# Kernel tuning notes

Measured on AMD Instinct MI355X. Metric: run time of the kernel, lower is better.

The kernel has to match this reference:

```python
import jax, jax.numpy as jnp
import numpy as np

N = 524288
B, F, H, W = 2, 4, 64, 512
S = B * F * H * W  # dense voxel segment space
EPS = 1e-5


def _bn(x, g, b):
    # BatchNorm1d in training mode: normalize over the point dim with biased var
    m = x.mean(0)
    v = jnp.mean((x - m) ** 2, 0)
    return (x - m) / jnp.sqrt(v + EPS) * g + b


def setup_inputs() -> dict:
    key = jax.random.key(0)
    ks = jax.random.split(key, 20)
    pts = jax.random.normal(ks[0], (N, 4), dtype=jnp.float32) * 10.0
    bcol = jax.random.randint(ks[1], (N, 1), 0, B)
    fcol = jax.random.randint(ks[2], (N, 1), 0, F)
    hcol = jax.random.randint(ks[3], (N, 1), 0, H)
    wcol = jax.random.randint(ks[4], (N, 1), 0, W)
    coors = jnp.concatenate([bcol, fcol, hcol, wcol], -1).astype(jnp.int32)
    # original reads batch_size/frame_size from coors[-1]
    coors = coors.at[-1].set(jnp.array([B - 1, F - 1, H - 1, W - 1], dtype=jnp.int32))
    s = 0.02
    p = {
        'pre_gamma': jnp.ones((8,), jnp.float32),
        'pre_beta': jnp.zeros((8,), jnp.float32),
        'W1': jax.random.normal(ks[5], (8, 64), jnp.float32) * s,
        'g1': jnp.ones((64,), jnp.float32), 'b1': jnp.zeros((64,), jnp.float32),
        'W2': jax.random.normal(ks[6], (64, 128), jnp.float32) * s,
        'g2': jnp.ones((128,), jnp.float32), 'b2': jnp.zeros((128,), jnp.float32),
        'W3': jax.random.normal(ks[7], (128, 256), jnp.float32) * s,
        'g3': jnp.ones((256,), jnp.float32), 'b3': jnp.zeros((256,), jnp.float32),
        'W4': jax.random.normal(ks[8], (256, 256), jnp.float32) * s,
        'b4': jnp.zeros((256,), jnp.float32),
        'Wc': jax.random.normal(ks[9], (256, 64), jnp.float32) * s,
        'bc': jnp.zeros((64,), jnp.float32),
    }
    return {'pts': pts, 'pts_coors': coors, **p}


def reference(pts, pts_coors, pre_gamma, pre_beta, W1, g1, b1, W2, g2, b2,
              W3, g3, b3, W4, b4, Wc, bc):
    c = pts_coors
    lin = ((c[:, 0] * F + c[:, 1]) * H + c[:, 2]) * W + c[:, 3]  # (N,)
    counts = jax.ops.segment_sum(jnp.ones((pts.shape[0],), pts.dtype), lin, num_segments=S)
    # with_distance
    dist = jnp.linalg.norm(pts[:, :3], axis=1, keepdims=True)
    # with_cluster_center: scatter_mean then gather
    vsum = jax.ops.segment_sum(pts, lin, num_segments=S)
    vmean = vsum / jnp.clip(counts, 1.0)[:, None]
    f_cluster = pts[:, :3] - vmean[lin][:, :3]
    feats = jnp.concatenate([pts, dist, f_cluster], -1)  # (N, 8)
    feats = _bn(feats, pre_gamma, pre_beta)  # pre_norm
    x = jax.nn.relu(_bn(feats @ W1, g1, b1))
    x = jax.nn.relu(_bn(x @ W2, g2, b2))
    x = jax.nn.relu(_bn(x @ W3, g3, b3))
    point_feats = x @ W4 + b4  # (N, 256)
    # scatter_max over voxels
    seg = jax.ops.segment_max(point_feats, lin, num_segments=S)
    mask = (counts > 0)[:, None]
    voxel_feats = jnp.where(mask, seg, 0.0)
    comp = jax.nn.relu(voxel_feats @ Wc + bc)
    comp = jnp.where(mask, comp, 0.0)  # empty voxels stay zero in stack_frame
    stack = comp.reshape(B, F, H, W, -1)  # (B, F, H, W, Cc)
    residual = jnp.concatenate([stack[:, -1] - stack[:, f] for f in range(F - 1)], -1)
    residual_img = jnp.transpose(residual, (0, 3, 1, 2))  # (B, C, H, W)
    return residual_img
```

## Files before the change

### kernel.cpp

```cpp
#include <hip/hip_runtime.h>
#include <hip/hip_bf16.h>
#include <stdint.h>

typedef unsigned int u32;
typedef unsigned short u16;
typedef __attribute__((ext_vector_type(8))) short bf16x8;
typedef __attribute__((ext_vector_type(4))) float f32x4;

#define NPTS 524288
#define FF 4
#define HH 64
#define WW 512
#define SS 262144
#define EPSV 1e-5f
#define NB 8192
#define RCAP 80
#define VCAP 80

__device__ __forceinline__ float bf2f(u16 h){ return __uint_as_float(((u32)h)<<16); }
__device__ __forceinline__ u16 f2bf(float f){
  u32 u = __float_as_uint(f);
  return (u16)((u + 0x7FFFu + ((u>>16)&1u)) >> 16);
}

__device__ __forceinline__ void point_feats(int p, const float* __restrict__ pts,
    const u32* __restrict__ lin, const u32* __restrict__ counts,
    const float* __restrict__ vsum, float f[8], u32* vout){
  float4 pt = ((const float4*)pts)[p];
  u32 v = lin[p];
  float cnt = fmaxf((float)counts[v], 1.0f);
  float inv = 1.0f/cnt;
  float mx = vsum[v*3+0]*inv, my = vsum[v*3+1]*inv, mz = vsum[v*3+2]*inv;
  float dist = sqrtf(pt.x*pt.x + pt.y*pt.y + pt.z*pt.z);
  f[0]=pt.x; f[1]=pt.y; f[2]=pt.z; f[3]=pt.w; f[4]=dist;
  f[5]=pt.x-mx; f[6]=pt.y-my; f[7]=pt.z-mz;
  *vout = v;
}

__global__ __launch_bounds__(256) void k_lin(const float* __restrict__ pts,
                                             const int* __restrict__ coors,
                                             u32* __restrict__ lin,
                                             u32* __restrict__ counts,
                                             float* __restrict__ vsum){
  int p = blockIdx.x*256 + threadIdx.x;
  int4 c = ((const int4*)coors)[p];
  u32 v = ((u32)((c.x*FF + c.y)*HH + c.z))*WW + (u32)c.w;
  lin[p] = v;
  atomicAdd(&counts[v], 1u);
  float4 pt = ((const float4*)pts)[p];
  atomicAdd(&vsum[v*3+0], pt.x);
  atomicAdd(&vsum[v*3+1], pt.y);
  atomicAdd(&vsum[v*3+2], pt.z);
}

__global__ __launch_bounds__(256) void k_scan_a(const u32* __restrict__ counts,
                                                u32* __restrict__ blockSums){
  __shared__ u32 lds[256];
  int b = blockIdx.x, t = threadIdx.x;
  uint4 c4 = ((const uint4*)counts)[b*256 + t];
  lds[t] = c4.x + c4.y + c4.z + c4.w;
  __syncthreads();
  for(int s=128; s>0; s>>=1){ if(t<s) lds[t] += lds[t+s]; __syncthreads(); }
  if(t==0) blockSums[b] = lds[0];
}

__global__ void k_scan_b(u32* blockSums){
  if(threadIdx.x==0){
    u32 run = 0;
    for(int i=0;i<256;i++){ u32 v = blockSums[i]; blockSums[i] = run; run += v; }
  }
}

__global__ __launch_bounds__(256) void k_scan_c(const u32* __restrict__ counts,
                                                const u32* __restrict__ blockSums,
                                                u32* __restrict__ offsets,
                                                u32* __restrict__ cursor){
  __shared__ u32 lds[256];
  int b = blockIdx.x, t = threadIdx.x;
  uint4 c4 = ((const uint4*)counts)[b*256 + t];
  u32 mysum = c4.x + c4.y + c4.z + c4.w;
  lds[t] = mysum;
  __syncthreads();
  for(int d=1; d<256; d<<=1){
    u32 v = (t>=d) ? lds[t-d] : 0u;
    __syncthreads();
    lds[t] += v;
    __syncthreads();
  }
  u32 off = blockSums[b] + (t>0 ? lds[t-1] : 0u);
  u32 base = (u32)(b*1024 + t*4);
  offsets[base+0]=off; cursor[base+0]=off; off += c4.x;
  offsets[base+1]=off; cursor[base+1]=off; off += c4.y;
  offsets[base+2]=off; cursor[base+2]=off; off += c4.z;
  offsets[base+3]=off; cursor[base+3]=off; off += c4.w;
  if(base+4 == SS) offsets[SS] = off;
}

__global__ __launch_bounds__(256) void k_scatter(const u32* __restrict__ lin,
                                                 u32* __restrict__ cursor,
                                                 u32* __restrict__ order){
  int p = blockIdx.x*256 + threadIdx.x;
  u32 v = lin[p];
  u32 pos = atomicAdd(&cursor[v], 1u);
  order[pos] = p;
}

__global__ __launch_bounds__(256) void k_prep(const float* __restrict__ W2,
    const float* __restrict__ W3, const float* __restrict__ W4,
    const float* __restrict__ Wc,
    u16* __restrict__ W2t, u16* __restrict__ W3t, u16* __restrict__ W4t,
    u16* __restrict__ Wct){
  int i = blockIdx.x*256 + threadIdx.x;
  if(i < 8192){
    int k = i >> 7, n = i & 127;
    W2t[n*64 + k] = f2bf(W2[i]);
  } else if(i < 8192+32768){
    int j = i - 8192;
    int k = j >> 8, n = j & 255;
    W3t[n*128 + k] = f2bf(W3[j]);
  } else if(i < 8192+32768+65536){
    int j = i - (8192+32768);
    int k = j >> 8, n = j & 255;
    W4t[n*256 + k] = f2bf(W4[j]);
  } else if(i < 8192+32768+65536+16384){
    int j = i - (8192+32768+65536);
    int k = j >> 6, n = j & 63;
    Wct[n*256 + k] = f2bf(Wc[j]);
  }
}

__global__ __launch_bounds__(256) void k_stats0(const float* __restrict__ pts,
    const u32* __restrict__ lin, const u32* __restrict__ counts,
    const float* __restrict__ vsum, float* __restrict__ sum0, float* __restrict__ sq0){
  int p = blockIdx.x*256 + threadIdx.x;
  float f[8]; u32 v;
  point_feats(p, pts, lin, counts, vsum, f, &v);
  __shared__ float lsum[4][8], lsq[4][8];
  int lane = threadIdx.x & 63, wv = threadIdx.x >> 6;
  #pragma unroll
  for(int c=0;c<8;c++){
    float s = f[c], q = f[c]*f[c];
    #pragma unroll
    for(int d=32; d; d>>=1){ s += __shfl_xor(s,d); q += __shfl_xor(q,d); }
    if(lane==0){ lsum[wv][c]=s; lsq[wv][c]=q; }
  }
  __syncthreads();
  if(threadIdx.x<8){
    float s=0.f,q=0.f;
    for(int g=0;g<4;g++){ s+=lsum[g][threadIdx.x]; q+=lsq[g][threadIdx.x]; }
    atomicAdd(&sum0[threadIdx.x], s);
    atomicAdd(&sq0[threadIdx.x], q);
  }
}

__global__ void k_fold(const float* __restrict__ sum, const float* __restrict__ sq,
                       const float* __restrict__ g, const float* __restrict__ b,
                       float* __restrict__ a, float* __restrict__ c, int C){
  int i = blockIdx.x*64 + threadIdx.x;
  if(i < C){
    float m = sum[i]*(1.0f/NPTS);
    float v = sq[i]*(1.0f/NPTS) - m*m;
    v = fmaxf(v, 0.0f);
    float ai = g[i] / sqrtf(v + EPSV);
    a[i] = ai;
    c[i] = b[i] - m*ai;
  }
}

__global__ __launch_bounds__(256) void k_stats1(const float* __restrict__ pts,
    const u32* __restrict__ lin, const u32* __restrict__ counts,
    const float* __restrict__ vsum,
    const float* __restrict__ a0, const float* __restrict__ c0,
    const float* __restrict__ W1, float* __restrict__ sum1, float* __restrict__ sq1){
  __shared__ float ws[4][64], wq[4][64];
  int t = threadIdx.x;
  int p = blockIdx.x*256 + t;
  float f[8]; u32 v;
  point_feats(p, pts, lin, counts, vsum, f, &v);
  float y0[8];
  #pragma unroll
  for(int k=0;k<8;k++) y0[k] = a0[k]*f[k] + c0[k];
  float z[64];
  #pragma unroll
  for(int j=0;j<64;j++){
    float s=0.f;
    #pragma unroll
    for(int k=0;k<8;k++) s += y0[k]*W1[k*64+j];
    z[j]=s;
  }
  int lane = t&63, wv = t>>6;
  float ks=0.f, kq=0.f;
  #pragma unroll
  for(int c=0;c<64;c++){
    float s=z[c], q=z[c]*z[c];
    #pragma unroll
    for(int d=1; d<64; d<<=1){ s+=__shfl_xor(s,d); q+=__shfl_xor(q,d); }
    if(lane==c){ ks=s; kq=q; }
  }
  ws[wv][lane]=ks; wq[wv][lane]=kq;
  __syncthreads();
  if(t<64){
    float S=ws[0][t]+ws[1][t]+ws[2][t]+ws[3][t];
    float Q=wq[0][t]+wq[1][t]+wq[2][t]+wq[3][t];
    atomicAdd(&sum1[t],S); atomicAdd(&sq1[t],Q);
  }
}

__global__ __launch_bounds__(256,2) void k_mstats2(
    const float* __restrict__ pts, const u32* __restrict__ lin,
    const u32* __restrict__ counts, const float* __restrict__ vsum,
    const float* __restrict__ a0, const float* __restrict__ c0,
    const float* __restrict__ a1, const float* __restrict__ c1,
    const float* __restrict__ W1, const u16* __restrict__ W2t,
    float* __restrict__ sum2, float* __restrict__ sq2){
  __shared__ u16 T1[256*72];
  int tid = threadIdx.x, lane = tid&63, wid = tid>>6, l15 = lane&15, lg = lane>>4;
  float s2[2] = {0.f,0.f}, q2[2] = {0.f,0.f};

  for(int cch=0; cch<4; cch++){
    int p = blockIdx.x*1024 + cch*256 + tid;
    float f[8]; u32 v;
    point_feats(p, pts, lin, counts, vsum, f, &v);
    float y0[8];
    #pragma unroll
    for(int k=0;k<8;k++) y0[k] = a0[k]*f[k] + c0[k];
    u32 pk[32];
    #pragma unroll
    for(int jj=0;jj<32;jj++){
      float s0=0.f, s1=0.f;
      #pragma unroll
      for(int k=0;k<8;k++){ s0 += y0[k]*W1[k*64+2*jj]; s1 += y0[k]*W1[k*64+2*jj+1]; }
      float v0f = fmaxf(a1[2*jj]*s0   + c1[2*jj],   0.f);
      float v1f = fmaxf(a1[2*jj+1]*s1 + c1[2*jj+1], 0.f);
      pk[jj] = (u32)f2bf(v0f) | ((u32)f2bf(v1f)<<16);
    }
    __syncthreads();
    {
      uint4* dst = (uint4*)&T1[tid*72];
      #pragma unroll
      for(int q=0;q<8;q++) dst[q] = make_uint4(pk[4*q],pk[4*q+1],pk[4*q+2],pk[4*q+3]);
    }
    __syncthreads();
    #pragma unroll
    for(int ci=0; ci<2; ci++){
      int ch = (wid + 4*ci)*16 + l15;
      const u16* wb = W2t + (size_t)ch*64 + lg*8;
      bf16x8 b0 = *(const bf16x8*)(wb);
      bf16x8 b1 = *(const bf16x8*)(wb + 32);
      for(int rt=0; rt<16; rt++){
        const u16* ap = T1 + (rt*16 + l15)*72 + lg*8;
        bf16x8 af0 = *(const bf16x8*)(ap);
        bf16x8 af1 = *(const bf16x8*)(ap + 32);
        f32x4 acc = {0.f,0.f,0.f,0.f};
        acc = __builtin_amdgcn_mfma_f32_16x16x32_bf16(af0, b0, acc, 0,0,0);
        acc = __builtin_amdgcn_mfma_f32_16x16x32_bf16(af1, b1, acc, 0,0,0);
        #pragma unroll
        for(int i=0;i<4;i++){ s2[ci] += acc[i]; q2[ci] += acc[i]*acc[i]; }
      }
    }
  }
  #pragma unroll
  for(int ci=0; ci<2; ci++){
    float s = s2[ci], q = q2[ci];
    s += __shfl_xor(s,16); s += __shfl_xor(s,32);
    q += __shfl_xor(q,16); q += __shfl_xor(q,32);
    if(lg == 0){
      int ch = (wid + 4*ci)*16 + l15;
      atomicAdd(&sum2[ch], s);
      atomicAdd(&sq2[ch], q);
    }
  }
}

__global__ __launch_bounds__(256,1) void k_chain2(
    const float* __restrict__ pts, const u32* __restrict__ lin,
    const u32* __restrict__ counts, const float* __restrict__ vsum,
    const u32* __restrict__ order,
    const float* __restrict__ a0, const float* __restrict__ c0,
    const float* __restrict__ a1, const float* __restrict__ c1,
    const float* __restrict__ a2, const float* __restrict__ c2,
    const float* __restrict__ W1, const u16* __restrict__ W2t,
    const u16* __restrict__ W3t,
    u32* __restrict__ y2s,
    float* __restrict__ sum3, float* __restrict__ sq3){
  __shared__ u16 T1[256*72];
  __shared__ u16 T2[256*136];
  int tid = threadIdx.x, lane = tid&63, wid = tid>>6, l15 = lane&15, lg = lane>>4;
  float s3[4] = {0.f,0.f,0.f,0.f}, q3[4] = {0.f,0.f,0.f,0.f};

  for(int cch=0; cch<4; cch++){
    int rr = blockIdx.x*1024 + cch*256 + tid;
    int p = (int)order[rr];
    float f[8]; u32 v;
    point_feats(p, pts, lin, counts, vsum, f, &v);
    float y0[8];
    #pragma unroll
    for(int k=0;k<8;k++) y0[k] = a0[k]*f[k] + c0[k];
    u32 pk[32];
    #pragma unroll
    for(int jj=0;jj<32;jj++){
      float s0=0.f, s1=0.f;
      #pragma unroll
      for(int k=0;k<8;k++){ s0 += y0[k]*W1[k*64+2*jj]; s1 += y0[k]*W1[k*64+2*jj+1]; }
      float v0f = fmaxf(a1[2*jj]*s0   + c1[2*jj],   0.f);
      float v1f = fmaxf(a1[2*jj+1]*s1 + c1[2*jj+1], 0.f);
      pk[jj] = (u32)f2bf(v0f) | ((u32)f2bf(v1f)<<16);
    }
    __syncthreads();
    {
      uint4* dst = (uint4*)&T1[tid*72];
      #pragma unroll
      for(int q=0;q<8;q++) dst[q] = make_uint4(pk[4*q],pk[4*q+1],pk[4*q+2],pk[4*q+3]);
    }
    __syncthreads();
    #pragma unroll
    for(int ci=0; ci<2; ci++){
      int ch = (wid + 4*ci)*16 + l15;
      const u16* wb = W2t + (size_t)ch*64 + lg*8;
      bf16x8 b0 = *(const bf16x8*)(wb);
      bf16x8 b1 = *(const bf16x8*)(wb + 32);
      float a2v = a2[ch], c2v = c2[ch];
      for(int rt=0; rt<16; rt++){
        const u16* ap = T1 + (rt*16 + l15)*72 + lg*8;
        bf16x8 af0 = *(const bf16x8*)(ap);
        bf16x8 af1 = *(const bf16x8*)(ap + 32);
        f32x4 acc = {0.f,0.f,0.f,0.f};
        acc = __builtin_amdgcn_mfma_f32_16x16x32_bf16(af0, b0, acc, 0,0,0);
        acc = __builtin_amdgcn_mfma_f32_16x16x32_bf16(af1, b1, acc, 0,0,0);
        int rbase = rt*16 + lg*4;
        #pragma unroll
        for(int i=0;i<4;i++)
          T2[(rbase+i)*136 + ch] = f2bf(fmaxf(a2v*acc[i] + c2v, 0.f));
      }
    }
    __syncthreads();
    {
      const u32* T2w = (const u32*)T2;
      u32 base = (u32)blockIdx.x*1024u + (u32)cch*256u;
      for(int i=tid; i<256*64; i+=256){
        int row = i>>6, w = i&63;
        y2s[(size_t)(base+row)*64 + w] = T2w[row*68 + w];
      }
    }
    #pragma unroll
    for(int ci=0; ci<4; ci++){
      int ch = (wid + 4*ci)*16 + l15;
      const u16* wb = W3t + (size_t)ch*128 + lg*8;
      bf16x8 b[4];
      #pragma unroll
      for(int ks=0; ks<4; ks++) b[ks] = *(const bf16x8*)(wb + ks*32);
      for(int rt=0; rt<16; rt++){
        const u16* ap = T2 + (rt*16 + l15)*136 + lg*8;
        f32x4 acc = {0.f,0.f,0.f,0.f};
        #pragma unroll
        for(int ks=0; ks<4; ks++){
          bf16x8 af = *(const bf16x8*)(ap + ks*32);
          acc = __builtin_amdgcn_mfma_f32_16x16x32_bf16(af, b[ks], acc, 0,0,0);
        }
        #pragma unroll
        for(int i=0;i<4;i++){ s3[ci] += acc[i]; q3[ci] += acc[i]*acc[i]; }
      }
    }
  }
  #pragma unroll
  for(int ci=0; ci<4; ci++){
    float s = s3[ci], q = q3[ci];
    s += __shfl_xor(s,16); s += __shfl_xor(s,32);
    q += __shfl_xor(q,16); q += __shfl_xor(q,32);
    if(lg == 0){
      int ch = (wid + 4*ci)*16 + l15;
      atomicAdd(&sum3[ch], s);
      atomicAdd(&sq3[ch], q);
    }
  }
}

__global__ __launch_bounds__(512,4) void k_mega5(
    const u32* __restrict__ offsets, const u32* __restrict__ y2s,
    const float* __restrict__ a3, const float* __restrict__ c3,
    const u16* __restrict__ W3t, const u16* __restrict__ W4t,
    const u16* __restrict__ Wct,
    const float* __restrict__ b4, const float* __restrict__ bc,
    u16* __restrict__ comp){
  __shared__ __align__(16) char SM[65664];
  u16* T3  = (u16*)(SM);
  u16* T2s = (u16*)(SM + 42240);
  u16* Tz  = (u16*)(SM + 42240);
  u16* TA  = (u16*)(SM + 53760);
  u32* vst = (u32*)(SM + 65280);
  u32* hdr = (u32*)(SM + 65616);

  int tid = threadIdx.x, lane = tid & 63, wid = tid >> 6;
  int l15 = lane & 15, lg = lane >> 4;
  int cg = wid & 3, rh = wid >> 2;
  int nvt = rh ? 2 : 3, vt0 = rh ? 3 : 0;

  if(tid == 0){
    u32 t0 = (u32)blockIdx.x * 64u;
    u32 lo=0, hi=SS;
    while(lo<hi){ u32 mid=(lo+hi)>>1; if(offsets[mid] < t0) lo=mid+1; else hi=mid; }
    u32 vlo = lo, vhi;
    if(blockIdx.x == NB-1) vhi = SS;
    else {
      u32 t1 = t0 + 64u;
      lo = vlo; hi = SS;
      while(lo<hi){ u32 mid=(lo+hi)>>1; if(offsets[mid] < t1) lo=mid+1; else hi=mid; }
      vhi = lo;
    }
    hdr[0]=vlo; hdr[1]=vhi; hdr[2]=offsets[vlo]; hdr[3]=offsets[vhi];
  }
  __syncthreads();
  u32 vlo=hdr[0], vhi=hdr[1], start=hdr[2], end=hdr[3];
  int R = (int)(end - start); if(R > RCAP) R = RCAP;
  int V = (int)(vhi - vlo);   if(V > VCAP) V = VCAP;

  if(tid <= VCAP){
    u32 o = (tid <= V) ? offsets[vlo + tid] : end;
    int s = (int)(o - start); if(s > RCAP) s = RCAP;
    vst[tid] = (u32)s;
  }

  {
    u32* T2w = (u32*)T2s;
    for(int i=tid; i<RCAP*64; i+=512){
      int row = i>>6, w = i&63;
      u32 val = (row < R) ? y2s[(size_t)(start+row)*64 + w] : 0u;
      T2w[row*68 + w] = val;
    }
  }
  __syncthreads();

  for(int ci=0; ci<2; ci++){
    int ch = (wid + 8*ci)*16 + l15;
    const u16* wb = W3t + (size_t)ch*128 + lg*8;
    bf16x8 b[4];
    #pragma unroll
    for(int ks=0; ks<4; ks++) b[ks] = *(const bf16x8*)(wb + ks*32);
    float a3v = a3[ch], c3v = c3[ch];
    for(int rt=0; rt<5; rt++){
      const u16* ap = T2s + (rt*16 + l15)*136 + lg*8;
      f32x4 acc = {0.f,0.f,0.f,0.f};
      #pragma unroll
      for(int ks=0; ks<4; ks++){
        bf16x8 af = *(const bf16x8*)(ap + ks*32);
        acc = __builtin_amdgcn_mfma_f32_16x16x32_bf16(af, b[ks], acc, 0,0,0);
      }
      int rbase = rt*16 + lg*4;
      #pragma unroll
      for(int i=0;i<4;i++)
        T3[(rbase+i)*264 + ch] = f2bf(fmaxf(a3v*acc[i] + c3v, 0.f));
    }
  }
  __syncthreads();

  f32x4 acc3[3];
  #pragma unroll
  for(int i=0;i<3;i++) acc3[i] = (f32x4){0.f,0.f,0.f,0.f};
  int ch4 = cg*16 + l15;

  for(int oc=0; oc<4; oc++){
    {
      int chg = oc*64 + ch4;
      const u16* wb = W4t + (size_t)chg*256 + lg*8;
      bf16x8 b[8];
      #pragma unroll
      for(int ks=0; ks<8; ks++) b[ks] = *(const bf16x8*)(wb + ks*32);
      int rtB = rh ? 3 : 0, rtE = rh ? 5 : 3;
      for(int rt=rtB; rt<rtE; rt++){
        const u16* ap = T3 + (rt*16 + l15)*264 + lg*8;
        f32x4 acc = {0.f,0.f,0.f,0.f};
        #pragma unroll
        for(int ks=0; ks<8; ks++){
          bf16x8 af = *(const bf16x8*)(ap + ks*32);
          acc = __builtin_amdgcn_mfma_f32_16x16x32_bf16(af, b[ks], acc, 0,0,0);
        }
        int rbase = rt*16 + lg*4;
        #pragma unroll
        for(int i=0;i<4;i++)
          Tz[(rbase+i)*72 + ch4] = f2bf(acc[i]);
      }
    }
    __syncthreads();
    for(int i=tid; i<VCAP*64; i+=512){
      int v = i>>6, k = i&63;
      u32 r0 = vst[v], r1 = vst[v+1];
      u16 outv = 0;
      if(r1 > r0){
        float m = -3.0e38f;
        for(u32 r=r0; r<r1; r++) m = fmaxf(m, bf2f(Tz[r*72+k]));
        outv = f2bf(m + b4[oc*64+k]);
      }
      TA[v*72+k] = outv;
    }
    __syncthreads();
    {
      const u16* wb = Wct + (size_t)ch4*256 + oc*64 + lg*8;
      bf16x8 b0 = *(const bf16x8*)(wb);
      bf16x8 b1 = *(const bf16x8*)(wb + 32);
      #pragma unroll
      for(int s=0; s<3; s++){
        if(s < nvt){
          int vt = vt0 + s;
          const u16* ap = TA + (vt*16 + l15)*72 + lg*8;
          bf16x8 af0 = *(const bf16x8*)(ap);
          bf16x8 af1 = *(const bf16x8*)(ap + 32);
          acc3[s] = __builtin_amdgcn_mfma_f32_16x16x32_bf16(af0, b0, acc3[s], 0,0,0);
          acc3[s] = __builtin_amdgcn_mfma_f32_16x16x32_bf16(af1, b1, acc3[s], 0,0,0);
        }
      }
    }
  }

  {
    float bcv = bc[ch4];
    #pragma unroll
    for(int s=0; s<3; s++){
      if(s < nvt){
        int vt = vt0 + s;
        int vbase = vt*16 + lg*4;
        #pragma unroll
        for(int i=0;i<4;i++){
          int vox = vbase + i;
          if(vox < V){
            bool nz = vst[vox+1] > vst[vox];
            float val = nz ? fmaxf(acc3[s][i] + bcv, 0.f) : 0.f;
            comp[(size_t)(vlo+vox)*64 + ch4] = f2bf(val);
          }
        }
      }
    }
  }
}

__global__ __launch_bounds__(256) void k_resid(const u16* __restrict__ comp,
                                               float* __restrict__ out){
  __shared__ u32 cl[4*128*32];
  int t = threadIdx.x;
  int blk = blockIdx.x;
  int wq = blk & 3, h = (blk>>2) & 63, b = blk>>8;
  int w0 = wq*128;
  for(int fr=0; fr<4; fr++){
    const u32* src = (const u32*)comp + ((size_t)(((b*4+fr)*64 + h)*512 + w0))*32;
    for(int i=t; i<4096; i+=256){
      int vox = i>>5, wd = i&31;
      cl[fr*4096 + vox*32 + (wd ^ (vox&31))] = src[i];
    }
  }
  __syncthreads();
  int wl = t & 127, half = t >> 7;
  int mv = wl & 31;
  for(int ch = half; ch < 64; ch += 2){
    u32 wr3 = cl[3*4096 + wl*32 + ((ch>>1) ^ mv)];
    float r3 = bf2f((ch&1) ? (u16)(wr3>>16) : (u16)(wr3&0xFFFFu));
    #pragma unroll
    for(int fr=0; fr<3; fr++){
      u32 wrf = cl[fr*4096 + wl*32 + ((ch>>1) ^ mv)];
      float vf = bf2f((ch&1) ? (u16)(wrf>>16) : (u16)(wrf&0xFFFFu));
      out[(((size_t)(b*192 + fr*64 + ch))*64 + h)*512 + w0 + wl] = r3 - vf;
    }
  }
}

extern "C" void kernel_launch(void* const* d_in, const int* in_sizes, int n_in,
                              void* d_out, int out_size, void* d_ws, size_t ws_size,
                              hipStream_t stream){
  const float* pts  = (const float*)d_in[0];
  const int*  coors = (const int*)d_in[1];
  const float* g0 = (const float*)d_in[2];
  const float* b0 = (const float*)d_in[3];
  const float* W1 = (const float*)d_in[4];
  const float* g1 = (const float*)d_in[5];
  const float* b1 = (const float*)d_in[6];
  const float* W2 = (const float*)d_in[7];
  const float* g2 = (const float*)d_in[8];
  const float* b2 = (const float*)d_in[9];
  const float* W3 = (const float*)d_in[10];
  const float* g3 = (const float*)d_in[11];
  const float* b3 = (const float*)d_in[12];
  const float* W4 = (const float*)d_in[13];
  const float* b4 = (const float*)d_in[14];
  const float* Wc = (const float*)d_in[15];
  const float* bc = (const float*)d_in[16];
  float* out = (float*)d_out;
  (void)in_sizes; (void)n_in; (void)out_size; (void)ws_size;

  char* ws = (char*)d_ws;
  size_t off = 0;
  auto alloc = [&](size_t bytes)->void*{
    void* p = ws + off;
    off += (bytes + 255) & ~(size_t)255;
    return p;
  };
  u32*  counts  = (u32*)alloc((size_t)SS*4);
  float* vsum   = (float*)alloc((size_t)SS*3*4);
  float* stats  = (float*)alloc(8192);
  size_t zero_bytes = off;
  u32*  lin     = (u32*)alloc((size_t)NPTS*4);
  u32*  offsets = (u32*)alloc((size_t)(SS+1)*4);
  u32*  cursor  = (u32*)alloc((size_t)SS*4);
  u32*  order   = (u32*)alloc((size_t)NPTS*4);
  u32*  blockSums = (u32*)alloc(1024);
  u16*  comp    = (u16*)alloc((size_t)SS*64*2);
  u16*  W2t = (u16*)alloc(8192*2);
  u16*  W3t = (u16*)alloc(32768*2);
  u16*  W4t = (u16*)alloc(65536*2);
  u16*  Wct = (u16*)alloc(16384*2);
  u32*  y2s = (u32*)alloc((size_t)NPTS*64*4);

  float* sum0=stats+0,   *sq0=stats+8,    *a0=stats+16,   *c0=stats+24;
  float* sum1=stats+32,  *sq1=stats+96,   *a1=stats+160,  *c1=stats+224;
  float* sum2=stats+288, *sq2=stats+416,  *a2=stats+544,  *c2=stats+672;
  float* sum3=stats+800, *sq3=stats+1056, *a3=stats+1312, *c3=stats+1568;

  hipMemsetAsync(d_ws, 0, zero_bytes, stream);

  k_prep   <<<480, 256,0,stream>>>(W2, W3, W4, Wc, W2t, W3t, W4t, Wct);
  k_lin    <<<2048,256,0,stream>>>(pts, coors, lin, counts, vsum);
  k_scan_a <<<256, 256,0,stream>>>(counts, blockSums);
  k_scan_b <<<1,   64, 0,stream>>>(blockSums);
  k_scan_c <<<256, 256,0,stream>>>(counts, blockSums, offsets, cursor);
  k_scatter<<<2048,256,0,stream>>>(lin, cursor, order);

  k_stats0 <<<2048,256,0,stream>>>(pts, lin, counts, vsum, sum0, sq0);
  k_fold   <<<1,   64, 0,stream>>>(sum0, sq0, g0, b0, a0, c0, 8);
  k_stats1 <<<2048,256,0,stream>>>(pts, lin, counts, vsum, a0, c0, W1, sum1, sq1);
  k_fold   <<<1,   64, 0,stream>>>(sum1, sq1, g1, b1, a1, c1, 64);
  k_mstats2<<<512, 256,0,stream>>>(pts, lin, counts, vsum, a0,c0,a1,c1, W1, W2t, sum2, sq2);
  k_fold   <<<2,   64, 0,stream>>>(sum2, sq2, g2, b2, a2, c2, 128);
  k_chain2 <<<512, 256,0,stream>>>(pts, lin, counts, vsum, order,
                                   a0,c0,a1,c1,a2,c2, W1, W2t, W3t,
                                   y2s, sum3, sq3);
  k_fold   <<<4,   64, 0,stream>>>(sum3, sq3, g3, b3, a3, c3, 256);

  k_mega5  <<<NB,  512,0,stream>>>(offsets, y2s, a3,c3, W3t, W4t, Wct, b4, bc, comp);
  k_resid  <<<512, 256,0,stream>>>(comp, out);
}
```

Before: 1.106 ms.

## Process W4 output chunks in pairs to reuse A-fragments and halve sync passes

The W4 GEMM stage in the mega kernel now computes two 64-channel output chunks per pass, loading each T3 A-fragment once and feeding two MFMA accumulators, with results written to two separate LDS staging buffers. Segment-max and the compression GEMM then run for each chunk in turn. The b4 bias is also staged in LDS. The aim is fewer LDS reads of T3 and fewer outer-loop barrier rounds. In exchange, LDS use grows to about 78KB per block and register pressure roughly doubles for the B fragments, which may lower occupancy. The extra barriers added per chunk also offset part of the saved synchronisation.

```diff
diff --git a/kernel.cpp b/kernel.cpp
--- a/kernel.cpp
+++ b/kernel.cpp
@@ -375,20 +375,22 @@
   }
 }
 
-__global__ __launch_bounds__(512,4) void k_mega5(
+__global__ __launch_bounds__(512,4) void k_mega6(
     const u32* __restrict__ offsets, const u32* __restrict__ y2s,
     const float* __restrict__ a3, const float* __restrict__ c3,
     const u16* __restrict__ W3t, const u16* __restrict__ W4t,
     const u16* __restrict__ Wct,
     const float* __restrict__ b4, const float* __restrict__ bc,
     u16* __restrict__ comp){
-  __shared__ __align__(16) char SM[65664];
+  __shared__ __align__(16) char SM[78208];
   u16* T3  = (u16*)(SM);
   u16* T2s = (u16*)(SM + 42240);
-  u16* Tz  = (u16*)(SM + 42240);
-  u16* TA  = (u16*)(SM + 53760);
-  u32* vst = (u32*)(SM + 65280);
-  u32* hdr = (u32*)(SM + 65616);
+  u16* Tz0 = (u16*)(SM + 42240);
+  u16* Tz1 = (u16*)(SM + 53760);
+  u16* TA  = (u16*)(SM + 65280);
+  u32* vst = (u32*)(SM + 76800);
+  float* bb = (float*)(SM + 77152);
+  u32* hdr = (u32*)(SM + 78176);
 
   int tid = threadIdx.x, lane = tid & 63, wid = tid >> 6;
   int l15 = lane & 15, lg = lane >> 4;
@@ -409,6 +411,7 @@
     }
     hdr[0]=vlo; hdr[1]=vhi; hdr[2]=offsets[vlo]; hdr[3]=offsets[vhi];
   }
+  if(tid < 256) bb[tid] = b4[tid];
   __syncthreads();
   u32 vlo=hdr[0], vhi=hdr[1], start=hdr[2], end=hdr[3];
   int R = (int)(end - start); if(R > RCAP) R = RCAP;
@@ -458,26 +461,33 @@
   for(int i=0;i<3;i++) acc3[i] = (f32x4){0.f,0.f,0.f,0.f};
   int ch4 = cg*16 + l15;
 
-  for(int oc=0; oc<4; oc++){
+  for(int pr=0; pr<2; pr++){
+    int oc0 = 2*pr, oc1 = 2*pr + 1;
     {
-      int chg = oc*64 + ch4;
-      const u16* wb = W4t + (size_t)chg*256 + lg*8;
-      bf16x8 b[8];
-      #pragma unroll
-      for(int ks=0; ks<8; ks++) b[ks] = *(const bf16x8*)(wb + ks*32);
+      const u16* wb0 = W4t + (size_t)(oc0*64 + ch4)*256 + lg*8;
+      const u16* wb1 = W4t + (size_t)(oc1*64 + ch4)*256 + lg*8;
+      bf16x8 b0[8], b1[8];
+      #pragma unroll
+      for(int ks=0; ks<8; ks++){
+        b0[ks] = *(const bf16x8*)(wb0 + ks*32);
+        b1[ks] = *(const bf16x8*)(wb1 + ks*32);
+      }
       int rtB = rh ? 3 : 0, rtE = rh ? 5 : 3;
       for(int rt=rtB; rt<rtE; rt++){
         const u16* ap = T3 + (rt*16 + l15)*264 + lg*8;
-        f32x4 acc = {0.f,0.f,0.f,0.f};
+        f32x4 aA = {0.f,0.f,0.f,0.f}, aB = {0.f,0.f,0.f,0.f};
         #pragma unroll
         for(int ks=0; ks<8; ks++){
           bf16x8 af = *(const bf16x8*)(ap + ks*32);
-          acc = __builtin_amdgcn_mfma_f32_16x16x32_bf16(af, b[ks], acc, 0,0,0);
+          aA = __builtin_amdgcn_mfma_f32_16x16x32_bf16(af, b0[ks], aA, 0,0,0);
+          aB = __builtin_amdgcn_mfma_f32_16x16x32_bf16(af, b1[ks], aB, 0,0,0);
         }
         int rbase = rt*16 + lg*4;
         #pragma unroll
-        for(int i=0;i<4;i++)
-          Tz[(rbase+i)*72 + ch4] = f2bf(acc[i]);
+        for(int i=0;i<4;i++){
+          Tz0[(rbase+i)*72 + ch4] = f2bf(aA[i]);
+          Tz1[(rbase+i)*72 + ch4] = f2bf(aB[i]);
+        }
       }
     }
     __syncthreads();
@@ -487,16 +497,16 @@
       u16 outv = 0;
       if(r1 > r0){
         float m = -3.0e38f;
-        for(u32 r=r0; r<r1; r++) m = fmaxf(m, bf2f(Tz[r*72+k]));
-        outv = f2bf(m + b4[oc*64+k]);
+        for(u32 r=r0; r<r1; r++) m = fmaxf(m, bf2f(Tz0[r*72+k]));
+        outv = f2bf(m + bb[oc0*64+k]);
       }
       TA[v*72+k] = outv;
     }
     __syncthreads();
     {
-      const u16* wb = Wct + (size_t)ch4*256 + oc*64 + lg*8;
-      bf16x8 b0 = *(const bf16x8*)(wb);
-      bf16x8 b1 = *(const bf16x8*)(wb + 32);
+      const u16* wb = Wct + (size_t)ch4*256 + oc0*64 + lg*8;
+      bf16x8 c0f = *(const bf16x8*)(wb);
+      bf16x8 c1f = *(const bf16x8*)(wb + 32);
       #pragma unroll
       for(int s=0; s<3; s++){
         if(s < nvt){
@@ -504,11 +514,41 @@
           const u16* ap = TA + (vt*16 + l15)*72 + lg*8;
           bf16x8 af0 = *(const bf16x8*)(ap);
           bf16x8 af1 = *(const bf16x8*)(ap + 32);
-          acc3[s] = __builtin_amdgcn_mfma_f32_16x16x32_bf16(af0, b0, acc3[s], 0,0,0);
-          acc3[s] = __builtin_amdgcn_mfma_f32_16x16x32_bf16(af1, b1, acc3[s], 0,0,0);
+          acc3[s] = __builtin_amdgcn_mfma_f32_16x16x32_bf16(af0, c0f, acc3[s], 0,0,0);
+          acc3[s] = __builtin_amdgcn_mfma_f32_16x16x32_bf16(af1, c1f, acc3[s], 0,0,0);
         }
       }
     }
+    __syncthreads();
+    for(int i=tid; i<VCAP*64; i+=512){
+      int v = i>>6, k = i&63;
+      u32 r0 = vst[v], r1 = vst[v+1];
+      u16 outv = 0;
+      if(r1 > r0){
+        float m = -3.0e38f;
+        for(u32 r=r0; r<r1; r++) m = fmaxf(m, bf2f(Tz1[r*72+k]));
+        outv = f2bf(m + bb[oc1*64+k]);
+      }
+      TA[v*72+k] = outv;
+    }
+    __syncthreads();
+    {
+      const u16* wb = Wct + (size_t)ch4*256 + oc1*64 + lg*8;
+      bf16x8 c0f = *(const bf16x8*)(wb);
+      bf16x8 c1f = *(const bf16x8*)(wb + 32);
+      #pragma unroll
+      for(int s=0; s<3; s++){
+        if(s < nvt){
+          int vt = vt0 + s;
+          const u16* ap = TA + (vt*16 + l15)*72 + lg*8;
+          bf16x8 af0 = *(const bf16x8*)(ap);
+          bf16x8 af1 = *(const bf16x8*)(ap + 32);
+          acc3[s] = __builtin_amdgcn_mfma_f32_16x16x32_bf16(af0, c0f, acc3[s], 0,0,0);
+          acc3[s] = __builtin_amdgcn_mfma_f32_16x16x32_bf16(af1, c1f, acc3[s], 0,0,0);
+        }
+      }
+    }
+    __syncthreads();
   }
 
   {
@@ -632,6 +672,6 @@
                                    y2s, sum3, sq3);
   k_fold   <<<4,   64, 0,stream>>>(sum3, sq3, g3, b3, a3, c3, 256);
 
-  k_mega5  <<<NB,  512,0,stream>>>(offsets, y2s, a3,c3, W3t, W4t, Wct, b4, bc, comp);
+  k_mega6  <<<NB,  512,0,stream>>>(offsets, y2s, a3,c3, W3t, W4t, Wct, b4, bc, comp);
   k_resid  <<<512, 256,0,stream>>>(comp, out);
 }
```

Result: no change. 1.092 ms (-1.2%).
